# Kernel tuning notes

Measured on AMD Instinct MI355X. Metric: run time of the kernel, lower is better.

Reference implementation:

```python
import jax, jax.numpy as jnp
import numpy as np

C = 32
RES = 512
LEVEL = 6
RADIUS = 2  # half-width of specular filtering window per mip level
_lev_res = [RES >> i for i in range(LEVEL)]
_offsets = np.concatenate([[0], np.cumsum([r * r for r in _lev_res])]).astype(np.int32)
TOTAL = int(_offsets[-1])
_roughness = np.linspace(0.03, 0.99, LEVEL).astype(np.float32)


def _face_dirs(R):
    # unit direction of each texel center on each of the 6 cube faces: (6,R,R,3)
    t = ((np.arange(R) + 0.5) / R * 2.0 - 1.0).astype(np.float32)
    vv, uu = np.meshgrid(t, t, indexing='ij')  # vv: rows (v), uu: cols (u)
    one = np.ones_like(uu)
    f = np.stack([
        np.stack([one, -vv, -uu], -1),   # +x
        np.stack([-one, -vv, uu], -1),   # -x
        np.stack([uu, one, vv], -1),     # +y
        np.stack([uu, -one, -vv], -1),   # -y
        np.stack([uu, -vv, one], -1),    # +z
        np.stack([-uu, -vv, -one], -1)], 0)  # -z
    return (f / np.linalg.norm(f, axis=-1, keepdims=True)).astype(np.float32)

_DIRS = [jnp.asarray(_face_dirs(r)) for r in _lev_res]


def _ggx(cos, alpha):
    a2 = alpha * alpha
    d = a2 / (np.pi * (cos * cos * (a2 - 1.0) + 1.0) ** 2)
    return jnp.where(cos > 0, d, 0.0)


def _specular_filter(feat, dirs, rough):
    # GGX-weighted neighborhood filtering per texel (bounded window = 'specular bound')
    R = feat.shape[-1]
    alpha = float(rough) ** 2
    idx = jnp.arange(R)
    fsum = jnp.zeros_like(feat)
    wsum = jnp.zeros(feat.shape[1:], dtype=feat.dtype)  # (6,R,R)
    for di in range(-RADIUS, RADIUS + 1):
        ii = jnp.clip(idx + di, 0, R - 1)
        for dj in range(-RADIUS, RADIUS + 1):
            jj = jnp.clip(idx + dj, 0, R - 1)
            nd = dirs[:, ii][:, :, jj]                    # (6,R,R,3)
            cos = jnp.clip((dirs * nd).sum(-1), -1.0, 1.0)
            wgt = _ggx(cos, alpha)                        # (6,R,R)
            fsum = fsum + feat[:, :, ii][:, :, :, jj] * wgt[None]
            wsum = wsum + wgt
    return fsum / jnp.maximum(wsum, 1e-8)[None]


def _avg_pool2(x):
    Cc, F, R, _ = x.shape
    return x.reshape(Cc, F, R // 2, 2, R // 2, 2).mean(axis=(3, 5))


def _create_mip(feature):
    pools = [feature.reshape(C, 6, -1)]
    feat = feature
    for i in range(1, LEVEL):
        feat = _avg_pool2(feat)
        pools.append(_specular_filter(feat, _DIRS[i], float(_roughness[i])).reshape(C, 6, -1))
    return jnp.concatenate(pools, axis=-1)  # (C, 6, TOTAL)


def _fetch(mip_pool, w, r):
    # w in [0,1] encodes direction d = 2w-1; pick major-axis cube face, bilinear in face,
    # linear across mip levels selected by roughness r.
    d = w * 2.0 - 1.0
    d = d / jnp.linalg.norm(d, axis=-1, keepdims=True)
    dx, dy, dz = d[:, 0], d[:, 1], d[:, 2]
    ax, ay, az = jnp.abs(dx), jnp.abs(dy), jnp.abs(dz)
    condx = (ax >= ay) & (ax >= az)
    condy = (ay >= az) & (~condx)
    ma = jnp.where(condx, ax, jnp.where(condy, ay, az))
    face = jnp.where(condx, jnp.where(dx > 0, 0, 1),
           jnp.where(condy, jnp.where(dy > 0, 2, 3), jnp.where(dz > 0, 4, 5)))
    u = jnp.where(condx, jnp.where(dx > 0, -dz, dz),
        jnp.where(condy, dx, jnp.where(dz > 0, dx, -dx))) / ma
    v = jnp.where(condx, -dy, jnp.where(condy, jnp.where(dy > 0, dz, -dz), -dy)) / ma
    u01 = (u + 1.0) * 0.5
    v01 = (v + 1.0) * 0.5
    lev_f = jnp.clip((r - _roughness[0]) / (_roughness[-1] - _roughness[0]), 0.0, 1.0) * (LEVEL - 1)
    l0 = jnp.clip(jnp.floor(lev_f).astype(jnp.int32), 0, LEVEL - 1)
    l1 = jnp.minimum(l0 + 1, LEVEL - 1)
    t = lev_f - l0.astype(lev_f.dtype)
    offs = jnp.asarray(_offsets)
    pool_flat = mip_pool.reshape(C, 6 * TOTAL)
    fbase = face.astype(jnp.int32) * TOTAL

    def sample(l):
        res_l = (RES // jnp.left_shift(1, l)).astype(jnp.int32)  # per-query level res
        rf = res_l.astype(u01.dtype)
        x = jnp.clip(u01 * rf - 0.5, 0.0, rf - 1.0)
        y = jnp.clip(v01 * rf - 0.5, 0.0, rf - 1.0)
        x0 = jnp.floor(x).astype(jnp.int32)
        y0 = jnp.floor(y).astype(jnp.int32)
        x1 = jnp.minimum(x0 + 1, res_l - 1)
        y1 = jnp.minimum(y0 + 1, res_l - 1)
        fx = x - x0
        fy = y - y0
        base = fbase + offs[l]
        def g(yy, xx):
            return jnp.take(pool_flat, base + yy * res_l + xx, axis=1)  # (C,B)
        return (g(y0, x0) * (1 - fx) * (1 - fy) + g(y0, x1) * fx * (1 - fy)
              + g(y1, x0) * (1 - fx) * fy + g(y1, x1) * fx * fy)

    out = sample(l0) * (1 - t) + sample(l1) * t  # (C,B)
    return out.T  # (B,C)


def setup_inputs() -> dict:
    key = jax.random.key(0)
    k1, k2, k3 = jax.random.split(key, 3)
    B = 262144
    feature = jax.random.normal(k1, (C, 6, RES, RES), dtype=jnp.float32) * 0.1
    w = jax.random.uniform(k2, (B, 3), dtype=jnp.float32)
    r = jax.random.uniform(k3, (B,), dtype=jnp.float32)
    return {"feature": feature, "w": w, "r": r}


def reference(feature, w, r):
    mip_pool = _create_mip(feature)
    return _fetch(mip_pool, w, r)
```

## Files before the change

kernel.cpp:

```cpp
#include <hip/hip_runtime.h>
#include <cstddef>

#define PI_F 3.14159265358979323846f
#define TOTAL_TEX 349440
#define NC 32

__constant__ int c_offs[6] = {0, 262144, 327680, 344064, 348160, 349184};

__global__ __launch_bounds__(256) void k_transpose_pool(
    const float* __restrict__ feat, float* __restrict__ pool_t,
    float* __restrict__ pooled1)
{
  __shared__ float tile[256 * 33];
  int blk = blockIdx.x;
  int f = blk >> 10;
  int t = blk & 1023;
  int gy0 = (t >> 5) << 4;
  int gx0 = (t & 31) << 4;
  int tid = threadIdx.x;
  int ly = tid >> 4, lx = tid & 15;

  for (int c = 0; c < NC; ++c) {
    tile[(ly * 16 + lx) * 33 + c] =
        feat[(((size_t)c * 6 + f) * 512 + (gy0 + ly)) * 512 + (gx0 + lx)];
  }
  __syncthreads();

  size_t base0 = ((size_t)f * TOTAL_TEX + (size_t)gy0 * 512 + gx0) * NC;
  for (int it = 0; it < 32; ++it) {
    int e = it * 256 + tid;
    int c = e & 31;
    int x = (e >> 5) & 15;
    int y = e >> 9;
    pool_t[base0 + ((size_t)y * 512 + x) * NC + c] = tile[(y * 16 + x) * 33 + c];
  }

  size_t base1 = ((size_t)f * 65536 + (size_t)(gy0 >> 1) * 256 + (gx0 >> 1)) * NC;
  for (int it = 0; it < 8; ++it) {
    int e = it * 256 + tid;
    int c = e & 31;
    int x1 = (e >> 5) & 7;
    int y1 = e >> 8;
    float v = 0.25f * ((tile[((2 * y1) * 16 + 2 * x1) * 33 + c] +
                        tile[((2 * y1) * 16 + 2 * x1 + 1) * 33 + c]) +
                       (tile[((2 * y1 + 1) * 16 + 2 * x1) * 33 + c] +
                        tile[((2 * y1 + 1) * 16 + 2 * x1 + 1) * 33 + c]));
    pooled1[base1 + ((size_t)y1 * 256 + x1) * NC + c] = v;
  }
}

__global__ __launch_bounds__(256) void k_pool(
    const float* __restrict__ in, float* __restrict__ out,
    int Rin, int logRout, int n)
{
  int t = blockIdx.x * 256 + threadIdx.x;
  if (t >= n) return;
  int c = t & 31;
  int rem = t >> 5;
  int Rout = Rin >> 1;
  int x = rem & (Rout - 1);
  rem >>= logRout;
  int y = rem & (Rout - 1);
  int f = rem >> logRout;
  size_t b = (((size_t)f * Rin + 2 * y) * Rin + 2 * x) * NC + c;
  size_t rowstep = (size_t)Rin * NC;
  out[t] = 0.25f * ((in[b] + in[b + NC]) + (in[b + rowstep] + in[b + rowstep + NC]));
}

__device__ inline float3 face_dir_norm(int f, int i, int j, float inv2R)
{
  float u = ((float)j + 0.5f) * inv2R - 1.0f;
  float v = ((float)i + 0.5f) * inv2R - 1.0f;
  float x, y, z;
  switch (f) {
    case 0: x = 1.0f;  y = -v; z = -u;   break;
    case 1: x = -1.0f; y = -v; z = u;    break;
    case 2: x = u;  y = 1.0f;  z = v;    break;
    case 3: x = u;  y = -1.0f; z = -v;   break;
    case 4: x = u;  y = -v;    z = 1.0f; break;
    default: x = -u; y = -v;   z = -1.0f; break;
  }
  float s = 1.0f / sqrtf(x * x + y * y + z * z);
  float3 o; o.x = x * s; o.y = y * s; o.z = z * s;
  return o;
}

__global__ __launch_bounds__(256) void k_filter2(
    const float* __restrict__ in, float* __restrict__ out,
    int R, int logR, float a2)
{
  __shared__ float wlds[32 * 26];
  int tid = threadIdx.x;
  int p0 = blockIdx.x << 5;
  float inv2R = 2.0f / (float)R;

  {
    int pl = tid & 31;
    int tg = tid >> 5;
    int p = p0 + pl;
    int j = p & (R - 1);
    int i = (p >> logR) & (R - 1);
    int f = p >> (2 * logR);
    float3 dc = face_dir_norm(f, i, j, inv2R);
    for (int tap = tg; tap < 25; tap += 8) {
      int di = tap / 5 - 2;
      int dj = tap - (tap / 5) * 5 - 2;
      int ii = min(max(i + di, 0), R - 1);
      int jj = min(max(j + dj, 0), R - 1);
      float3 dn = face_dir_norm(f, ii, jj, inv2R);
      float cs = dc.x * dn.x + dc.y * dn.y + dc.z * dn.z;
      cs = fminf(fmaxf(cs, -1.0f), 1.0f);
      float den = cs * cs * (a2 - 1.0f) + 1.0f;
      float w = (cs > 0.0f) ? (a2 / (PI_F * den * den)) : 0.0f;
      wlds[pl * 26 + tap] = w;
    }
  }
  __syncthreads();

  int cg = tid & 7;
  int pl = tid >> 3;
  int p = p0 + pl;
  int j = p & (R - 1);
  int i = (p >> logR) & (R - 1);
  int f = p >> (2 * logR);
  const float4* fbase = (const float4*)(in + (((size_t)f << (2 * logR)) * NC));

  float4 acc; acc.x = acc.y = acc.z = acc.w = 0.0f;
  float wsum = 0.0f;
#pragma unroll
  for (int di = -2; di <= 2; ++di) {
    int ii = min(max(i + di, 0), R - 1);
    int rowb = ii * R;
#pragma unroll
    for (int dj = -2; dj <= 2; ++dj) {
      int jj = min(max(j + dj, 0), R - 1);
      int tap = (di + 2) * 5 + (dj + 2);
      float w = wlds[pl * 26 + tap];
      wsum += w;
      float4 v = fbase[(size_t)(rowb + jj) * 8 + cg];
      acc.x += w * v.x; acc.y += w * v.y; acc.z += w * v.z; acc.w += w * v.w;
    }
  }
  float s = 1.0f / fmaxf(wsum, 1e-8f);
  float4 q; q.x = acc.x * s; q.y = acc.y * s; q.z = acc.z * s; q.w = acc.w * s;
  float4* o = (float4*)(out + ((size_t)f * TOTAL_TEX + (size_t)(i * R + j)) * NC);
  o[cg] = q;
}

__global__ __launch_bounds__(256) void k_fetch2(
    const float* __restrict__ pool_t, const float* __restrict__ wv,
    const float* __restrict__ rv, float* __restrict__ out, int B)
{
  int t = blockIdx.x * 256 + threadIdx.x;
  int cg = t & 7;
  int b = t >> 3;
  if (b >= B) return;

  float dx = wv[3 * b + 0] * 2.0f - 1.0f;
  float dy = wv[3 * b + 1] * 2.0f - 1.0f;
  float dz = wv[3 * b + 2] * 2.0f - 1.0f;
  float ax = fabsf(dx), ay = fabsf(dy), az = fabsf(dz);
  bool condx = (ax >= ay) && (ax >= az);
  bool condy = (ay >= az) && !condx;
  float ma = condx ? ax : (condy ? ay : az);
  int face = condx ? (dx > 0.0f ? 0 : 1)
                   : (condy ? (dy > 0.0f ? 2 : 3) : (dz > 0.0f ? 4 : 5));
  float un = condx ? (dx > 0.0f ? -dz : dz)
                   : (condy ? dx : (dz > 0.0f ? dx : -dx));
  float vn = condx ? -dy : (condy ? (dy > 0.0f ? dz : -dz) : -dy);
  float u01 = (un / ma + 1.0f) * 0.5f;
  float v01 = (vn / ma + 1.0f) * 0.5f;

  float rr = rv[b];
  float lev_f = fminf(fmaxf((rr - 0.03f) / (0.99f - 0.03f), 0.0f), 1.0f) * 5.0f;
  int l0 = (int)floorf(lev_f);
  l0 = min(max(l0, 0), 5);
  int l1 = min(l0 + 1, 5);
  float tt = lev_f - (float)l0;

  float4 acc; acc.x = acc.y = acc.z = acc.w = 0.0f;
  int   lvs[2] = {l0, l1};
  float lws[2] = {1.0f - tt, tt};
#pragma unroll
  for (int s = 0; s < 2; ++s) {
    int l = lvs[s];
    float wl = lws[s];
    int res = 512 >> l;
    float rf = (float)res;
    float x = fminf(fmaxf(u01 * rf - 0.5f, 0.0f), rf - 1.0f);
    float y = fminf(fmaxf(v01 * rf - 0.5f, 0.0f), rf - 1.0f);
    int x0 = (int)floorf(x), y0 = (int)floorf(y);
    int x1 = min(x0 + 1, res - 1), y1 = min(y0 + 1, res - 1);
    float fx = x - (float)x0, fy = y - (float)y0;
    const float4* base4 =
        (const float4*)(pool_t + ((size_t)face * TOTAL_TEX + c_offs[l]) * NC);
    float w00 = wl * (1.0f - fx) * (1.0f - fy);
    float w01 = wl * fx * (1.0f - fy);
    float w10 = wl * (1.0f - fx) * fy;
    float w11 = wl * fx * fy;
    float4 a = base4[(size_t)(y0 * res + x0) * 8 + cg];
    float4 bq = base4[(size_t)(y0 * res + x1) * 8 + cg];
    float4 cq = base4[(size_t)(y1 * res + x0) * 8 + cg];
    float4 dq = base4[(size_t)(y1 * res + x1) * 8 + cg];
    acc.x += w00 * a.x + w01 * bq.x + w10 * cq.x + w11 * dq.x;
    acc.y += w00 * a.y + w01 * bq.y + w10 * cq.y + w11 * dq.y;
    acc.z += w00 * a.z + w01 * bq.z + w10 * cq.z + w11 * dq.z;
    acc.w += w00 * a.w + w01 * bq.w + w10 * cq.w + w11 * dq.w;
  }
  ((float4*)(out + (size_t)b * NC))[cg] = acc;
}

extern "C" void kernel_launch(void* const* d_in, const int* in_sizes, int n_in,
                              void* d_out, int out_size, void* d_ws, size_t ws_size,
                              hipStream_t stream)
{
  const float* feat = (const float*)d_in[0];
  const float* wv   = (const float*)d_in[1];
  const float* rv   = (const float*)d_in[2];
  float* out = (float*)d_out;
  int B = in_sizes[1] / 3;

  float* pool_t = (float*)d_ws;
  const size_t POOLT = (size_t)6 * TOTAL_TEX * NC;
  float* pooled1 = pool_t + POOLT;
  float* pooled2 = pooled1 + (size_t)6 * 256 * 256 * NC;
  float* pooled3 = pooled2 + (size_t)6 * 128 * 128 * NC;
  float* pooled4 = pooled3 + (size_t)6 * 64 * 64 * NC;
  float* pooled5 = pooled4 + (size_t)6 * 32 * 32 * NC;
  float* pooled[6] = {nullptr, pooled1, pooled2, pooled3, pooled4, pooled5};
  static const int offs[6] = {0, 262144, 327680, 344064, 348160, 349184};

  hipLaunchKernelGGL(k_transpose_pool, dim3(6 * 1024), dim3(256), 0, stream,
                     feat, pool_t, pooled1);

  for (int l = 2; l <= 5; ++l) {
    int Rin = 512 >> (l - 1);
    int Rout = 512 >> l;
    int logRout = 9 - l;
    int n = 6 * Rout * Rout * NC;
    hipLaunchKernelGGL(k_pool, dim3((n + 255) / 256), dim3(256), 0, stream,
                       pooled[l - 1], pooled[l], Rin, logRout, n);
  }

  for (int l = 1; l <= 5; ++l) {
    int R = 512 >> l;
    int logR = 9 - l;
    double rough_d = 0.03 + 0.192 * (double)l;
    float r32 = (float)rough_d;
    double alpha = (double)r32 * (double)r32;
    float a2 = (float)(alpha * alpha);
    int npix = 6 * R * R;
    hipLaunchKernelGGL(k_filter2, dim3(npix / 32), dim3(256), 0, stream,
                       pooled[l], pool_t + (size_t)offs[l] * NC, R, logR, a2);
  }

  hipLaunchKernelGGL(k_fetch2, dim3((B * 8 + 255) / 256), dim3(256), 0, stream,
                     pool_t, wv, rv, out, B);
}
```

Measured before the change: 481.9 us.

## Store mip pool in bf16 and retile transpose for coalesced row reads

Measured after the change: 443.7 us. -7.9%, faster.

```diff
diff --git a/kernel.cpp b/kernel.cpp
--- a/kernel.cpp
+++ b/kernel.cpp
@@ -4,48 +4,72 @@
 #define PI_F 3.14159265358979323846f
 #define TOTAL_TEX 349440
 #define NC 32
+#define LP 257
 
 __constant__ int c_offs[6] = {0, 262144, 327680, 344064, 348160, 349184};
 
+static __device__ inline unsigned int f2bf(float x) {
+  union { float f; unsigned int u; } v; v.f = x;
+  return (v.u + 0x7FFFu + ((v.u >> 16) & 1u)) >> 16;
+}
+static __device__ inline unsigned int pack2(float lo, float hi) {
+  return f2bf(lo) | (f2bf(hi) << 16);
+}
+static __device__ inline float4 bf4(uint2 q) {
+  union { unsigned int u; float f; } a;
+  float4 r;
+  a.u = q.x << 16;          r.x = a.f;
+  a.u = q.x & 0xFFFF0000u;  r.y = a.f;
+  a.u = q.y << 16;          r.z = a.f;
+  a.u = q.y & 0xFFFF0000u;  r.w = a.f;
+  return r;
+}
+
 __global__ __launch_bounds__(256) void k_transpose_pool(
-    const float* __restrict__ feat, float* __restrict__ pool_t,
+    const float* __restrict__ feat, unsigned short* __restrict__ pool0,
     float* __restrict__ pooled1)
 {
-  __shared__ float tile[256 * 33];
+  __shared__ float tile[32 * LP];
   int blk = blockIdx.x;
-  int f = blk >> 10;
-  int t = blk & 1023;
-  int gy0 = (t >> 5) << 4;
-  int gx0 = (t & 31) << 4;
+  int tx = blk & 7;
+  int rem = blk >> 3;
+  int ty = rem & 127;
+  int f = rem >> 7;
+  int gx0 = tx << 6, gy0 = ty << 2;
   int tid = threadIdx.x;
-  int ly = tid >> 4, lx = tid & 15;
-
-  for (int c = 0; c < NC; ++c) {
-    tile[(ly * 16 + lx) * 33 + c] =
-        feat[(((size_t)c * 6 + f) * 512 + (gy0 + ly)) * 512 + (gx0 + lx)];
+  int lx = tid & 63, ly = tid >> 6;
+  int pix = ly * 64 + lx;
+
+  const float* fp = feat + ((size_t)f * 512 + (gy0 + ly)) * 512 + gx0 + lx;
+#pragma unroll
+  for (int c = 0; c < 32; ++c) {
+    tile[c * LP + pix] = fp[(size_t)c * (6 * 512 * 512)];
   }
   __syncthreads();
 
-  size_t base0 = ((size_t)f * TOTAL_TEX + (size_t)gy0 * 512 + gx0) * NC;
-  for (int it = 0; it < 32; ++it) {
-    int e = it * 256 + tid;
-    int c = e & 31;
-    int x = (e >> 5) & 15;
-    int y = e >> 9;
-    pool_t[base0 + ((size_t)y * 512 + x) * NC + c] = tile[(y * 16 + x) * 33 + c];
-  }
-
-  size_t base1 = ((size_t)f * 65536 + (size_t)(gy0 >> 1) * 256 + (gx0 >> 1)) * NC;
+  size_t rowbase = ((size_t)f * TOTAL_TEX + (size_t)gy0 * 512 + gx0) * NC;
+#pragma unroll
+  for (int it = 0; it < 8; ++it) {
+    int q = it * 256 + tid;
+    int texel = q >> 3, cg = q & 7;
+    int tyy = texel >> 6, txx = texel & 63;
+    float v0 = tile[(cg * 4 + 0) * LP + texel];
+    float v1 = tile[(cg * 4 + 1) * LP + texel];
+    float v2 = tile[(cg * 4 + 2) * LP + texel];
+    float v3 = tile[(cg * 4 + 3) * LP + texel];
+    uint2 pk; pk.x = pack2(v0, v1); pk.y = pack2(v2, v3);
+    *(uint2*)(pool0 + rowbase + ((size_t)tyy * 512 + txx) * NC + cg * 4) = pk;
+  }
+
+  size_t pbase = ((size_t)f * 65536 + (size_t)(gy0 >> 1) * 256 + (gx0 >> 1)) * NC;
+#pragma unroll
   for (int it = 0; it < 8; ++it) {
     int e = it * 256 + tid;
-    int c = e & 31;
-    int x1 = (e >> 5) & 7;
-    int y1 = e >> 8;
-    float v = 0.25f * ((tile[((2 * y1) * 16 + 2 * x1) * 33 + c] +
-                        tile[((2 * y1) * 16 + 2 * x1 + 1) * 33 + c]) +
-                       (tile[((2 * y1 + 1) * 16 + 2 * x1) * 33 + c] +
-                        tile[((2 * y1 + 1) * 16 + 2 * x1 + 1) * 33 + c]));
-    pooled1[base1 + ((size_t)y1 * 256 + x1) * NC + c] = v;
+    int c = e & 31, px = (e >> 5) & 31, py = e >> 10;
+    int b0 = (2 * py) * 64 + 2 * px;
+    float v = 0.25f * ((tile[c * LP + b0] + tile[c * LP + b0 + 1]) +
+                       (tile[c * LP + b0 + 64] + tile[c * LP + b0 + 65]));
+    pooled1[pbase + ((size_t)py * 256 + px) * NC + c] = v;
   }
 }
 
@@ -86,7 +110,7 @@
 }
 
 __global__ __launch_bounds__(256) void k_filter2(
-    const float* __restrict__ in, float* __restrict__ out,
+    const float* __restrict__ in, unsigned short* __restrict__ out,
     int R, int logR, float a2)
 {
   __shared__ float wlds[32 * 26];
@@ -142,13 +166,14 @@
     }
   }
   float s = 1.0f / fmaxf(wsum, 1e-8f);
-  float4 q; q.x = acc.x * s; q.y = acc.y * s; q.z = acc.z * s; q.w = acc.w * s;
-  float4* o = (float4*)(out + ((size_t)f * TOTAL_TEX + (size_t)(i * R + j)) * NC);
-  o[cg] = q;
+  uint2 pk;
+  pk.x = pack2(acc.x * s, acc.y * s);
+  pk.y = pack2(acc.z * s, acc.w * s);
+  ((uint2*)(out + ((size_t)f * TOTAL_TEX + (size_t)(i * R + j)) * NC))[cg] = pk;
 }
 
 __global__ __launch_bounds__(256) void k_fetch2(
-    const float* __restrict__ pool_t, const float* __restrict__ wv,
+    const unsigned short* __restrict__ pool, const float* __restrict__ wv,
     const float* __restrict__ rv, float* __restrict__ out, int B)
 {
   int t = blockIdx.x * 256 + threadIdx.x;
@@ -192,16 +217,16 @@
     int x0 = (int)floorf(x), y0 = (int)floorf(y);
     int x1 = min(x0 + 1, res - 1), y1 = min(y0 + 1, res - 1);
     float fx = x - (float)x0, fy = y - (float)y0;
-    const float4* base4 =
-        (const float4*)(pool_t + ((size_t)face * TOTAL_TEX + c_offs[l]) * NC);
+    const uint2* base8 =
+        (const uint2*)(pool + ((size_t)face * TOTAL_TEX + c_offs[l]) * NC);
     float w00 = wl * (1.0f - fx) * (1.0f - fy);
     float w01 = wl * fx * (1.0f - fy);
     float w10 = wl * (1.0f - fx) * fy;
     float w11 = wl * fx * fy;
-    float4 a = base4[(size_t)(y0 * res + x0) * 8 + cg];
-    float4 bq = base4[(size_t)(y0 * res + x1) * 8 + cg];
-    float4 cq = base4[(size_t)(y1 * res + x0) * 8 + cg];
-    float4 dq = base4[(size_t)(y1 * res + x1) * 8 + cg];
+    float4 a = bf4(base8[(size_t)(y0 * res + x0) * 8 + cg]);
+    float4 bq = bf4(base8[(size_t)(y0 * res + x1) * 8 + cg]);
+    float4 cq = bf4(base8[(size_t)(y1 * res + x0) * 8 + cg]);
+    float4 dq = bf4(base8[(size_t)(y1 * res + x1) * 8 + cg]);
     acc.x += w00 * a.x + w01 * bq.x + w10 * cq.x + w11 * dq.x;
     acc.y += w00 * a.y + w01 * bq.y + w10 * cq.y + w11 * dq.y;
     acc.z += w00 * a.z + w01 * bq.z + w10 * cq.z + w11 * dq.z;
@@ -220,9 +245,9 @@
   float* out = (float*)d_out;
   int B = in_sizes[1] / 3;
 
-  float* pool_t = (float*)d_ws;
+  unsigned short* pool_t = (unsigned short*)d_ws;
   const size_t POOLT = (size_t)6 * TOTAL_TEX * NC;
-  float* pooled1 = pool_t + POOLT;
+  float* pooled1 = (float*)(pool_t + POOLT);
   float* pooled2 = pooled1 + (size_t)6 * 256 * 256 * NC;
   float* pooled3 = pooled2 + (size_t)6 * 128 * 128 * NC;
   float* pooled4 = pooled3 + (size_t)6 * 64 * 64 * NC;
@@ -230,7 +255,7 @@
   float* pooled[6] = {nullptr, pooled1, pooled2, pooled3, pooled4, pooled5};
   static const int offs[6] = {0, 262144, 327680, 344064, 348160, 349184};
 
-  hipLaunchKernelGGL(k_transpose_pool, dim3(6 * 1024), dim3(256), 0, stream,
+  hipLaunchKernelGGL(k_transpose_pool, dim3(6 * 8 * 128), dim3(256), 0, stream,
                      feat, pool_t, pooled1);
 
   for (int l = 2; l <= 5; ++l) {
```
